# Optimization experiments

Measured on AMD Instinct MI355X. Metric: run time of the kernel, lower is better.

## Reference

```python
import jax, jax.numpy as jnp
import numpy as np

N_GENES = 768
HID = 128


def setup_inputs() -> dict:
    key = jax.random.key(0)
    ks = jax.random.split(key, 7)
    s1 = 1.0 / np.sqrt(2 * HID)
    s2 = 1.0 / np.sqrt(HID)
    return {
        "gene_embeddings": jax.random.normal(ks[0], (N_GENES, HID), jnp.float32),
        # regulatory_classifier: Linear(2h -> h), ReLU, Linear(h -> 3)
        "W1": jax.random.normal(ks[1], (HID, 2 * HID), jnp.float32) * s1,
        "b1": jax.random.normal(ks[2], (HID,), jnp.float32) * s1,
        "W2": jax.random.normal(ks[3], (3, HID), jnp.float32) * s2,
        "b2": jax.random.normal(ks[4], (3,), jnp.float32) * s2,
        # binding_predictor: Bilinear(h, h, 1) -> weight [1, h, h], bias [1]
        "Wb": jax.random.normal(ks[5], (1, HID, HID), jnp.float32) * s2,
        "bb": jax.random.normal(ks[6], (1,), jnp.float32) * s2,
    }


def reference(gene_embeddings, W1, b1, W2, b2, Wb, bb):
    """Vectorized equivalent of GeneRegulatoryNetwork.compute_regulatory_matrix.

    For every ordered pair (i, j), i != j:
      logits   = MLP(cat[x_i, x_j])            -> [3]
      cls      = argmax(logits)
      affinity = x_i^T Wb x_j + bb             (nn.Bilinear, out=1)
      reg[i,j] = +affinity if cls==0, -affinity if cls==2, else 0
    """
    X = gene_embeddings  # [n, h]
    n, h = X.shape
    # Linear(2h -> h) on cat[x_i, x_j] splits into two per-gene projections.
    Ai = X @ W1[:, :h].T  # [n, h] contribution of gene_i
    Bj = X @ W1[:, h:].T  # [n, h] contribution of gene_j
    hidden = jax.nn.relu(Ai[:, None, :] + Bj[None, :, :] + b1)  # [n, n, h]
    logits = hidden @ W2.T + b2  # [n, n, 3]
    reg_class = jnp.argmax(logits, axis=-1)  # [n, n] (first-max, matches torch)
    # Bilinear affinity: x_i^T Wb[0] x_j + bb[0]
    affinity = jnp.einsum('ik,kl,jl->ij', X, Wb[0], X) + bb[0]  # [n, n]
    sign = jnp.where(reg_class == 0, 1.0, jnp.where(reg_class == 2, -1.0, 0.0))
    reg = (sign * affinity).astype(X.dtype)
    # i == j pairs are skipped in the original loop -> zero diagonal
    reg = reg * (1.0 - jnp.eye(n, dtype=reg.dtype))
    return reg
```

## Files before the change

kernel.cpp:

```cpp
#include <hip/hip_runtime.h>

#define N_GENES 768
#define H 128
#define TILE 48
#define LDP 132
#define LDPH 136

typedef float    f2 __attribute__((ext_vector_type(2)));
typedef _Float16 h2 __attribute__((ext_vector_type(2)));
typedef _Float16 h8 __attribute__((ext_vector_type(8)));

__global__ __launch_bounds__(128) void grn_pre(
    const float* __restrict__ X, const float* __restrict__ W1,
    const float* __restrict__ b1, const float* __restrict__ Wb,
    float* __restrict__ AiB, float* __restrict__ Bjp,
    _Float16* __restrict__ Yh, _Float16* __restrict__ Xh)
{
    const int m  = threadIdx.x;
    const int g0 = blockIdx.x * 3;

    __shared__ float Xs[3][H];
    #pragma unroll
    for (int r = 0; r < 3; ++r) Xs[r][m] = X[(g0 + r) * H + m];
    __syncthreads();

    double aib[3] = {0, 0, 0}, bj[3] = {0, 0, 0}, y[3] = {0, 0, 0};
    const float4* W1a = (const float4*)(W1 + m * (2 * H));
    const float4* W1b = (const float4*)(W1 + m * (2 * H) + H);

    #pragma unroll 4
    for (int kq = 0; kq < H / 4; ++kq) {
        float4 wa = W1a[kq];
        float4 wb = W1b[kq];
        float wc[4];
        #pragma unroll
        for (int e = 0; e < 4; ++e) wc[e] = Wb[(kq * 4 + e) * H + m];
        const float* wae = &wa.x;
        const float* wbe = &wb.x;
        #pragma unroll
        for (int r = 0; r < 3; ++r) {
            float4 xr = *(const float4*)&Xs[r][kq * 4];
            const float* xe = &xr.x;
            #pragma unroll
            for (int e = 0; e < 4; ++e) {
                aib[r] += (double)xe[e] * (double)wae[e];
                bj[r]  += (double)xe[e] * (double)wbe[e];
                y[r]   += (double)xe[e] * (double)wc[e];
            }
        }
    }

    const double b1m = (double)b1[m];
    #pragma unroll
    for (int r = 0; r < 3; ++r) {
        AiB[(g0 + r) * H + m] = (float)(aib[r] + b1m);
        Bjp[(g0 + r) * H + m] = (float)bj[r];
        Yh [(g0 + r) * H + m] = (_Float16)(float)y[r];
        Xh [(g0 + r) * H + m] = (_Float16)Xs[r][m];
    }
}

__device__ __forceinline__ void load_tile_f32(float* __restrict__ dst,
                                              const float* __restrict__ src, int tx)
{
    #pragma unroll
    for (int t = 0; t < 6; ++t) {
        int idx = tx + t * 256;
        int row = idx >> 5;
        int c4  = idx & 31;
        *(float4*)&dst[row * LDP + c4 * 4] = *(const float4*)&src[row * H + c4 * 4];
    }
}

__device__ __forceinline__ void load_tile_f16(_Float16* __restrict__ dst,
                                              const _Float16* __restrict__ src, int tx)
{
    #pragma unroll
    for (int t = 0; t < 3; ++t) {
        int idx = tx + t * 256;
        int row = idx >> 4;
        int c8  = idx & 15;
        *(h8*)&dst[row * LDPH + c8 * 8] = *(const h8*)&src[row * H + c8 * 8];
    }
}

__device__ __forceinline__ h2 hpair(h8 v, int p) { h2 r; r.x = v[2*p]; r.y = v[2*p+1]; return r; }

__global__ __launch_bounds__(256) void grn_main(
    const float* __restrict__ AiB, const float* __restrict__ Bjp,
    const _Float16* __restrict__ Yh, const _Float16* __restrict__ Xh,
    const float* __restrict__ W2,  const float* __restrict__ b2,
    const float* __restrict__ bb,  float* __restrict__ out)
{
    const int gj = blockIdx.x & 15;
    const int gi = blockIdx.x >> 4;
    const int tx = threadIdx.x;
    const int it = tx >> 4;
    const int jt = tx & 15;

    __shared__ float sL[TILE * LDP];
    __shared__ float sR[TILE * LDP];
    __shared__ float sW[2 * H];

    _Float16* sLh = (_Float16*)sL;
    _Float16* sRh = (_Float16*)sR;

    load_tile_f16(sLh, Yh + gi * TILE * H, tx);
    load_tile_f16(sRh, Xh + gj * TILE * H, tx);
    if (tx < H) {
        sW[tx]     = W2[tx] - W2[2 * H + tx];
        sW[H + tx] = W2[tx] - W2[H + tx];
    }
    __syncthreads();

    float aff[3][3] = {};
    #pragma unroll 2
    for (int q = 0; q < H / 8; ++q) {
        h8 yv[3], xv[3];
        #pragma unroll
        for (int r = 0; r < 3; ++r) yv[r] = *(const h8*)&sLh[(it + 16 * r) * LDPH + q * 8];
        #pragma unroll
        for (int c = 0; c < 3; ++c) xv[c] = *(const h8*)&sRh[(jt + 16 * c) * LDPH + q * 8];
        #pragma unroll
        for (int r = 0; r < 3; ++r)
            #pragma unroll
            for (int c = 0; c < 3; ++c)
                #pragma unroll
                for (int p = 0; p < 4; ++p) {
#if __has_builtin(__builtin_amdgcn_fdot2)
                    aff[r][c] = __builtin_amdgcn_fdot2(hpair(yv[r], p), hpair(xv[c], p),
                                                       aff[r][c], false);
#else
                    h2 a = hpair(yv[r], p), b = hpair(xv[c], p);
                    aff[r][c] = fmaf((float)a.x, (float)b.x, aff[r][c]);
                    aff[r][c] = fmaf((float)a.y, (float)b.y, aff[r][c]);
#endif
                }
    }

    __syncthreads();

    load_tile_f32(sL, AiB + gi * TILE * H, tx);
    load_tile_f32(sR, Bjp + gj * TILE * H, tx);
    __syncthreads();

    const float u0 = b2[0] - b2[2];
    const float v0 = b2[0] - b2[1];
    float u[3][3], v[3][3];
    #pragma unroll
    for (int r = 0; r < 3; ++r)
        #pragma unroll
        for (int c = 0; c < 3; ++c) { u[r][c] = u0; v[r][c] = v0; }

    const f2 zero2 = {0.0f, 0.0f};
    #pragma unroll 4
    for (int mq = 0; mq < H / 4; ++mq) {
        float4 w0 = *(const float4*)&sW[mq * 4];
        float4 w1 = *(const float4*)&sW[H + mq * 4];
        float4 av[3], bv[3];
        #pragma unroll
        for (int r = 0; r < 3; ++r) av[r] = *(const float4*)&sL[(it + 16 * r) * LDP + mq * 4];
        #pragma unroll
        for (int c = 0; c < 3; ++c) bv[c] = *(const float4*)&sR[(jt + 16 * c) * LDP + mq * 4];
        #pragma unroll
        for (int r = 0; r < 3; ++r) {
            f2 a01 = {av[r].x, av[r].y};
            f2 a23 = {av[r].z, av[r].w};
            #pragma unroll
            for (int c = 0; c < 3; ++c) {
                f2 b01 = {bv[c].x, bv[c].y};
                f2 b23 = {bv[c].z, bv[c].w};
                f2 h01 = __builtin_elementwise_max(a01 + b01, zero2);
                f2 h23 = __builtin_elementwise_max(a23 + b23, zero2);
                float uu = u[r][c], vv = v[r][c];
                uu = fmaf(h01.x, w0.x, uu); vv = fmaf(h01.x, w1.x, vv);
                uu = fmaf(h01.y, w0.y, uu); vv = fmaf(h01.y, w1.y, vv);
                uu = fmaf(h23.x, w0.z, uu); vv = fmaf(h23.x, w1.z, vv);
                uu = fmaf(h23.y, w0.w, uu); vv = fmaf(h23.y, w1.w, vv);
                u[r][c] = uu; v[r][c] = vv;
            }
        }
    }

    const float bbv = bb[0];
    #pragma unroll
    for (int r = 0; r < 3; ++r) {
        const int i = gi * TILE + it + 16 * r;
        #pragma unroll
        for (int c = 0; c < 3; ++c) {
            const int j = gj * TILE + jt + 16 * c;
            float A = aff[r][c] + bbv;
            float uu = u[r][c], vv = v[r][c];
            float s = (uu >= 0.0f && vv >= 0.0f) ? A
                    : ((uu < 0.0f && uu < vv) ? -A : 0.0f);
            if (i == j) s = 0.0f;
            out[i * N_GENES + j] = s;
        }
    }
}

extern "C" void kernel_launch(void* const* d_in, const int* in_sizes, int n_in,
                              void* d_out, int out_size, void* d_ws, size_t ws_size,
                              hipStream_t stream)
{
    const float* X  = (const float*)d_in[0];
    const float* W1 = (const float*)d_in[1];
    const float* b1 = (const float*)d_in[2];
    const float* W2 = (const float*)d_in[3];
    const float* b2 = (const float*)d_in[4];
    const float* Wb = (const float*)d_in[5];
    const float* bb = (const float*)d_in[6];
    float* out = (float*)d_out;

    float* ws  = (float*)d_ws;
    float*     AiB = ws;
    float*     Bjp = ws + N_GENES * H;
    _Float16*  Yh  = (_Float16*)(ws + 2 * N_GENES * H);
    _Float16*  Xh  = (_Float16*)(ws + 2 * N_GENES * H) + N_GENES * H;

    grn_pre <<<N_GENES / 3, 128, 0, stream>>>(X, W1, b1, Wb, AiB, Bjp, Yh, Xh);
    grn_main<<<256,         256, 0, stream>>>(AiB, Bjp, Yh, Xh, W2, b2, bb, out);
}
```

Baseline: 89.27 us.

## Prefetch MLP tiles into registers during affinity loop; precompute W2 diffs in pre-kernel

The main kernel now issues the global loads for the AiB/Bjp tiles into registers before the fp16 affinity dot-product loop, then writes them to separate shared buffers afterwards. This overlaps that load latency with compute and removes one barrier. The W2 difference vectors are computed once in the pre-kernel and read straight from global memory instead of being staged in shared memory. The u/v accumulators are packed into 2-wide vector FMAs. In exchange, shared memory use roughly grows (separate buffers instead of aliased ones) and register pressure rises from the 12 prefetched float4 values, which may reduce occupancy.

```diff
diff --git a/kernel.cpp b/kernel.cpp
--- a/kernel.cpp
+++ b/kernel.cpp
@@ -13,11 +13,18 @@
 __global__ __launch_bounds__(128) void grn_pre(
     const float* __restrict__ X, const float* __restrict__ W1,
     const float* __restrict__ b1, const float* __restrict__ Wb,
+    const float* __restrict__ W2,
     float* __restrict__ AiB, float* __restrict__ Bjp,
-    _Float16* __restrict__ Yh, _Float16* __restrict__ Xh)
+    _Float16* __restrict__ Yh, _Float16* __restrict__ Xh,
+    float* __restrict__ W2u, float* __restrict__ W2v)
 {
     const int m  = threadIdx.x;
     const int g0 = blockIdx.x * 3;
+
+    if (blockIdx.x == 0) {
+        W2u[m] = W2[m] - W2[2 * H + m];
+        W2v[m] = W2[m] - W2[H + m];
+    }
 
     __shared__ float Xs[3][H];
     #pragma unroll
@@ -60,37 +67,14 @@
     }
 }
 
-__device__ __forceinline__ void load_tile_f32(float* __restrict__ dst,
-                                              const float* __restrict__ src, int tx)
-{
-    #pragma unroll
-    for (int t = 0; t < 6; ++t) {
-        int idx = tx + t * 256;
-        int row = idx >> 5;
-        int c4  = idx & 31;
-        *(float4*)&dst[row * LDP + c4 * 4] = *(const float4*)&src[row * H + c4 * 4];
-    }
-}
-
-__device__ __forceinline__ void load_tile_f16(_Float16* __restrict__ dst,
-                                              const _Float16* __restrict__ src, int tx)
-{
-    #pragma unroll
-    for (int t = 0; t < 3; ++t) {
-        int idx = tx + t * 256;
-        int row = idx >> 4;
-        int c8  = idx & 15;
-        *(h8*)&dst[row * LDPH + c8 * 8] = *(const h8*)&src[row * H + c8 * 8];
-    }
-}
-
 __device__ __forceinline__ h2 hpair(h8 v, int p) { h2 r; r.x = v[2*p]; r.y = v[2*p+1]; return r; }
 
 __global__ __launch_bounds__(256) void grn_main(
     const float* __restrict__ AiB, const float* __restrict__ Bjp,
     const _Float16* __restrict__ Yh, const _Float16* __restrict__ Xh,
-    const float* __restrict__ W2,  const float* __restrict__ b2,
-    const float* __restrict__ bb,  float* __restrict__ out)
+    const float* __restrict__ W2u, const float* __restrict__ W2v,
+    const float* __restrict__ b2,  const float* __restrict__ bb,
+    float* __restrict__ out)
 {
     const int gj = blockIdx.x & 15;
     const int gi = blockIdx.x >> 4;
@@ -98,19 +82,38 @@
     const int it = tx >> 4;
     const int jt = tx & 15;
 
-    __shared__ float sL[TILE * LDP];
-    __shared__ float sR[TILE * LDP];
-    __shared__ float sW[2 * H];
-
-    _Float16* sLh = (_Float16*)sL;
-    _Float16* sRh = (_Float16*)sR;
-
-    load_tile_f16(sLh, Yh + gi * TILE * H, tx);
-    load_tile_f16(sRh, Xh + gj * TILE * H, tx);
-    if (tx < H) {
-        sW[tx]     = W2[tx] - W2[2 * H + tx];
-        sW[H + tx] = W2[tx] - W2[H + tx];
-    }
+    __shared__ _Float16 sYh[TILE * LDPH];
+    __shared__ _Float16 sXh[TILE * LDPH];
+    __shared__ float    sA [TILE * LDP];
+    __shared__ float    sB [TILE * LDP];
+
+    {
+        const _Float16* srcY = Yh + gi * TILE * H;
+        const _Float16* srcX = Xh + gj * TILE * H;
+        #pragma unroll
+        for (int t = 0; t < 3; ++t) {
+            int idx = tx + t * 256;
+            int row = idx >> 4;
+            int c8  = idx & 15;
+            *(h8*)&sYh[row * LDPH + c8 * 8] = *(const h8*)&srcY[row * H + c8 * 8];
+            *(h8*)&sXh[row * LDPH + c8 * 8] = *(const h8*)&srcX[row * H + c8 * 8];
+        }
+    }
+
+    float4 aReg[6], bReg[6];
+    {
+        const float* srcA = AiB + gi * TILE * H;
+        const float* srcB = Bjp + gj * TILE * H;
+        #pragma unroll
+        for (int t = 0; t < 6; ++t) {
+            int idx = tx + t * 256;
+            int row = idx >> 5;
+            int c4  = idx & 31;
+            aReg[t] = *(const float4*)&srcA[row * H + c4 * 4];
+            bReg[t] = *(const float4*)&srcB[row * H + c4 * 4];
+        }
+    }
+
     __syncthreads();
 
     float aff[3][3] = {};
@@ -118,9 +121,9 @@
     for (int q = 0; q < H / 8; ++q) {
         h8 yv[3], xv[3];
         #pragma unroll
-        for (int r = 0; r < 3; ++r) yv[r] = *(const h8*)&sLh[(it + 16 * r) * LDPH + q * 8];
-        #pragma unroll
-        for (int c = 0; c < 3; ++c) xv[c] = *(const h8*)&sRh[(jt + 16 * c) * LDPH + q * 8];
+        for (int r = 0; r < 3; ++r) yv[r] = *(const h8*)&sYh[(it + 16 * r) * LDPH + q * 8];
+        #pragma unroll
+        for (int c = 0; c < 3; ++c) xv[c] = *(const h8*)&sXh[(jt + 16 * c) * LDPH + q * 8];
         #pragma unroll
         for (int r = 0; r < 3; ++r)
             #pragma unroll
@@ -138,30 +141,36 @@
                 }
     }
 
-    __syncthreads();
-
-    load_tile_f32(sL, AiB + gi * TILE * H, tx);
-    load_tile_f32(sR, Bjp + gj * TILE * H, tx);
+    #pragma unroll
+    for (int t = 0; t < 6; ++t) {
+        int idx = tx + t * 256;
+        int row = idx >> 5;
+        int c4  = idx & 31;
+        *(float4*)&sA[row * LDP + c4 * 4] = aReg[t];
+        *(float4*)&sB[row * LDP + c4 * 4] = bReg[t];
+    }
     __syncthreads();
 
     const float u0 = b2[0] - b2[2];
     const float v0 = b2[0] - b2[1];
-    float u[3][3], v[3][3];
+    f2 uv[3][3];
     #pragma unroll
     for (int r = 0; r < 3; ++r)
         #pragma unroll
-        for (int c = 0; c < 3; ++c) { u[r][c] = u0; v[r][c] = v0; }
-
+        for (int c = 0; c < 3; ++c) { uv[r][c].x = u0; uv[r][c].y = v0; }
+
+    const float4* w0p = (const float4*)W2u;
+    const float4* w1p = (const float4*)W2v;
     const f2 zero2 = {0.0f, 0.0f};
     #pragma unroll 4
     for (int mq = 0; mq < H / 4; ++mq) {
-        float4 w0 = *(const float4*)&sW[mq * 4];
-        float4 w1 = *(const float4*)&sW[H + mq * 4];
+        float4 w0 = w0p[mq];
+        float4 w1 = w1p[mq];
         float4 av[3], bv[3];
         #pragma unroll
-        for (int r = 0; r < 3; ++r) av[r] = *(const float4*)&sL[(it + 16 * r) * LDP + mq * 4];
-        #pragma unroll
-        for (int c = 0; c < 3; ++c) bv[c] = *(const float4*)&sR[(jt + 16 * c) * LDP + mq * 4];
+        for (int r = 0; r < 3; ++r) av[r] = *(const float4*)&sA[(it + 16 * r) * LDP + mq * 4];
+        #pragma unroll
+        for (int c = 0; c < 3; ++c) bv[c] = *(const float4*)&sB[(jt + 16 * c) * LDP + mq * 4];
         #pragma unroll
         for (int r = 0; r < 3; ++r) {
             f2 a01 = {av[r].x, av[r].y};
@@ -172,12 +181,12 @@
                 f2 b23 = {bv[c].z, bv[c].w};
                 f2 h01 = __builtin_elementwise_max(a01 + b01, zero2);
                 f2 h23 = __builtin_elementwise_max(a23 + b23, zero2);
-                float uu = u[r][c], vv = v[r][c];
-                uu = fmaf(h01.x, w0.x, uu); vv = fmaf(h01.x, w1.x, vv);
-                uu = fmaf(h01.y, w0.y, uu); vv = fmaf(h01.y, w1.y, vv);
-                uu = fmaf(h23.x, w0.z, uu); vv = fmaf(h23.x, w1.z, vv);
-                uu = fmaf(h23.y, w0.w, uu); vv = fmaf(h23.y, w1.w, vv);
-                u[r][c] = uu; v[r][c] = vv;
+                f2 acc = uv[r][c];
+                acc = __builtin_elementwise_fma((f2){h01.x, h01.x}, (f2){w0.x, w1.x}, acc);
+                acc = __builtin_elementwise_fma((f2){h01.y, h01.y}, (f2){w0.y, w1.y}, acc);
+                acc = __builtin_elementwise_fma((f2){h23.x, h23.x}, (f2){w0.z, w1.z}, acc);
+                acc = __builtin_elementwise_fma((f2){h23.y, h23.y}, (f2){w0.w, w1.w}, acc);
+                uv[r][c] = acc;
             }
         }
     }
@@ -190,7 +199,7 @@
         for (int c = 0; c < 3; ++c) {
             const int j = gj * TILE + jt + 16 * c;
             float A = aff[r][c] + bbv;
-            float uu = u[r][c], vv = v[r][c];
+            float uu = uv[r][c].x, vv = uv[r][c].y;
             float s = (uu >= 0.0f && vv >= 0.0f) ? A
                     : ((uu < 0.0f && uu < vv) ? -A : 0.0f);
             if (i == j) s = 0.0f;
@@ -216,8 +225,10 @@
     float*     AiB = ws;
     float*     Bjp = ws + N_GENES * H;
     _Float16*  Yh  = (_Float16*)(ws + 2 * N_GENES * H);
-    _Float16*  Xh  = (_Float16*)(ws + 2 * N_GENES * H) + N_GENES * H;
-
-    grn_pre <<<N_GENES / 3, 128, 0, stream>>>(X, W1, b1, Wb, AiB, Bjp, Yh, Xh);
-    grn_main<<<256,         256, 0, stream>>>(AiB, Bjp, Yh, Xh, W2, b2, bb, out);
+    _Float16*  Xh  = Yh + N_GENES * H;
+    float*     W2u = ws + 3 * N_GENES * H;
+    float*     W2v = W2u + H;
+
+    grn_pre <<<N_GENES / 3, 128, 0, stream>>>(X, W1, b1, Wb, W2, AiB, Bjp, Yh, Xh, W2u, W2v);
+    grn_main<<<256,         256, 0, stream>>>(AiB, Bjp, Yh, Xh, W2u, W2v, b2, bb, out);
 }
```

Measured after the change: 94.00 us. 1.05x slower.

## Compute bilinear affinity with MFMA, split pre-kernel K-loop, prefetch tiles into registers

Applied to the files above, without the earlier changes.

The bilinear affinity tile is now computed with 16x16x32 f16 MFMA instructions that read fp16 operands straight from global memory. The results are staged in a shared-memory tile, replacing the per-thread fdot2 loop over LDS. The AiB/Bjp tile loads are issued into registers before the MFMA work so their latency overlaps it. The pre-kernel now uses 256 threads and splits the K reduction in half, combining partial sums in shared memory to shorten the double-precision dependency chain. The cost is more shared memory, extra global reads without LDS reuse for the MFMA operands, and an added reduction sync.

```diff
diff --git a/kernel.cpp b/kernel.cpp
--- a/kernel.cpp
+++ b/kernel.cpp
@@ -4,42 +4,45 @@
 #define H 128
 #define TILE 48
 #define LDP 132
-#define LDPH 136
-
-typedef float    f2 __attribute__((ext_vector_type(2)));
-typedef _Float16 h2 __attribute__((ext_vector_type(2)));
+#define LDSA 50
+
+typedef float f32x4 __attribute__((ext_vector_type(4)));
 typedef _Float16 h8 __attribute__((ext_vector_type(8)));
 
-__global__ __launch_bounds__(128) void grn_pre(
+__global__ __launch_bounds__(256) void grn_pre(
     const float* __restrict__ X, const float* __restrict__ W1,
     const float* __restrict__ b1, const float* __restrict__ Wb,
     float* __restrict__ AiB, float* __restrict__ Bjp,
     _Float16* __restrict__ Yh, _Float16* __restrict__ Xh)
 {
-    const int m  = threadIdx.x;
+    const int tx = threadIdx.x;
+    const int m  = tx & 127;
+    const int h  = tx >> 7;
     const int g0 = blockIdx.x * 3;
 
-    __shared__ float Xs[3][H];
-    #pragma unroll
-    for (int r = 0; r < 3; ++r) Xs[r][m] = X[(g0 + r) * H + m];
+    __shared__ float  Xs[3 * H];
+    __shared__ double parts[3][3][H];
+
+    for (int idx = tx; idx < 3 * H; idx += 256) Xs[idx] = X[g0 * H + idx];
     __syncthreads();
 
     double aib[3] = {0, 0, 0}, bj[3] = {0, 0, 0}, y[3] = {0, 0, 0};
-    const float4* W1a = (const float4*)(W1 + m * (2 * H));
-    const float4* W1b = (const float4*)(W1 + m * (2 * H) + H);
+    const int kb = h * 64;
+    const float4* W1a = (const float4*)(W1 + m * (2 * H) + kb);
+    const float4* W1b = (const float4*)(W1 + m * (2 * H) + H + kb);
 
     #pragma unroll 4
-    for (int kq = 0; kq < H / 4; ++kq) {
+    for (int kq = 0; kq < 16; ++kq) {
         float4 wa = W1a[kq];
         float4 wb = W1b[kq];
         float wc[4];
         #pragma unroll
-        for (int e = 0; e < 4; ++e) wc[e] = Wb[(kq * 4 + e) * H + m];
+        for (int e = 0; e < 4; ++e) wc[e] = Wb[(kb + kq * 4 + e) * H + m];
         const float* wae = &wa.x;
         const float* wbe = &wb.x;
         #pragma unroll
         for (int r = 0; r < 3; ++r) {
-            float4 xr = *(const float4*)&Xs[r][kq * 4];
+            float4 xr = *(const float4*)&Xs[r * H + kb + kq * 4];
             const float* xe = &xr.x;
             #pragma unroll
             for (int e = 0; e < 4; ++e) {
@@ -50,41 +53,30 @@
         }
     }
 
-    const double b1m = (double)b1[m];
-    #pragma unroll
-    for (int r = 0; r < 3; ++r) {
-        AiB[(g0 + r) * H + m] = (float)(aib[r] + b1m);
-        Bjp[(g0 + r) * H + m] = (float)bj[r];
-        Yh [(g0 + r) * H + m] = (_Float16)(float)y[r];
-        Xh [(g0 + r) * H + m] = (_Float16)Xs[r][m];
+    if (h == 1) {
+        #pragma unroll
+        for (int r = 0; r < 3; ++r) {
+            parts[0][r][m] = aib[r];
+            parts[1][r][m] = bj[r];
+            parts[2][r][m] = y[r];
+        }
+    }
+    __syncthreads();
+
+    if (h == 0) {
+        const double b1m = (double)b1[m];
+        #pragma unroll
+        for (int r = 0; r < 3; ++r) {
+            double A = aib[r] + parts[0][r][m];
+            double B = bj[r]  + parts[1][r][m];
+            double Y = y[r]   + parts[2][r][m];
+            AiB[(g0 + r) * H + m] = (float)(A + b1m);
+            Bjp[(g0 + r) * H + m] = (float)B;
+            Yh [(g0 + r) * H + m] = (_Float16)(float)Y;
+            Xh [(g0 + r) * H + m] = (_Float16)Xs[r * H + m];
+        }
     }
 }
-
-__device__ __forceinline__ void load_tile_f32(float* __restrict__ dst,
-                                              const float* __restrict__ src, int tx)
-{
-    #pragma unroll
-    for (int t = 0; t < 6; ++t) {
-        int idx = tx + t * 256;
-        int row = idx >> 5;
-        int c4  = idx & 31;
-        *(float4*)&dst[row * LDP + c4 * 4] = *(const float4*)&src[row * H + c4 * 4];
-    }
-}
-
-__device__ __forceinline__ void load_tile_f16(_Float16* __restrict__ dst,
-                                              const _Float16* __restrict__ src, int tx)
-{
-    #pragma unroll
-    for (int t = 0; t < 3; ++t) {
-        int idx = tx + t * 256;
-        int row = idx >> 4;
-        int c8  = idx & 15;
-        *(h8*)&dst[row * LDPH + c8 * 8] = *(const h8*)&src[row * H + c8 * 8];
-    }
-}
-
-__device__ __forceinline__ h2 hpair(h8 v, int p) { h2 r; r.x = v[2*p]; r.y = v[2*p+1]; return r; }
 
 __global__ __launch_bounds__(256) void grn_main(
     const float* __restrict__ AiB, const float* __restrict__ Bjp,
@@ -97,51 +89,62 @@
     const int tx = threadIdx.x;
     const int it = tx >> 4;
     const int jt = tx & 15;
-
-    __shared__ float sL[TILE * LDP];
-    __shared__ float sR[TILE * LDP];
-    __shared__ float sW[2 * H];
-
-    _Float16* sLh = (_Float16*)sL;
-    _Float16* sRh = (_Float16*)sR;
-
-    load_tile_f16(sLh, Yh + gi * TILE * H, tx);
-    load_tile_f16(sRh, Xh + gj * TILE * H, tx);
+    const int wid = tx >> 6;
+    const int l   = tx & 63;
+
+    __shared__ float sA [TILE * LDP];
+    __shared__ float sB [TILE * LDP];
+    __shared__ float sW [2 * H];
+    __shared__ float sAff[TILE * LDSA];
+
     if (tx < H) {
         sW[tx]     = W2[tx] - W2[2 * H + tx];
         sW[H + tx] = W2[tx] - W2[H + tx];
     }
-    __syncthreads();
-
-    float aff[3][3] = {};
-    #pragma unroll 2
-    for (int q = 0; q < H / 8; ++q) {
-        h8 yv[3], xv[3];
-        #pragma unroll
-        for (int r = 0; r < 3; ++r) yv[r] = *(const h8*)&sLh[(it + 16 * r) * LDPH + q * 8];
-        #pragma unroll
-        for (int c = 0; c < 3; ++c) xv[c] = *(const h8*)&sRh[(jt + 16 * c) * LDPH + q * 8];
-        #pragma unroll
-        for (int r = 0; r < 3; ++r)
-            #pragma unroll
-            for (int c = 0; c < 3; ++c)
-                #pragma unroll
-                for (int p = 0; p < 4; ++p) {
-#if __has_builtin(__builtin_amdgcn_fdot2)
-                    aff[r][c] = __builtin_amdgcn_fdot2(hpair(yv[r], p), hpair(xv[c], p),
-                                                       aff[r][c], false);
-#else
-                    h2 a = hpair(yv[r], p), b = hpair(xv[c], p);
-                    aff[r][c] = fmaf((float)a.x, (float)b.x, aff[r][c]);
-                    aff[r][c] = fmaf((float)a.y, (float)b.y, aff[r][c]);
-#endif
-                }
-    }
-
-    __syncthreads();
-
-    load_tile_f32(sL, AiB + gi * TILE * H, tx);
-    load_tile_f32(sR, Bjp + gj * TILE * H, tx);
+
+    float4 aReg[6], bReg[6];
+    {
+        const float* srcA = AiB + gi * TILE * H;
+        const float* srcB = Bjp + gj * TILE * H;
+        #pragma unroll
+        for (int t = 0; t < 6; ++t) {
+            int idx = tx + t * 256;
+            int row = idx >> 5;
+            int c4  = idx & 31;
+            aReg[t] = *(const float4*)&srcA[row * H + c4 * 4];
+            bReg[t] = *(const float4*)&srcB[row * H + c4 * 4];
+        }
+    }
+
+    {
+        const _Float16* Ybase = Yh + (gi * TILE) * H;
+        const _Float16* Xbase = Xh + (gj * TILE) * H;
+        const int ro = l & 15;
+        const int ko = (l >> 4) * 8;
+        for (int t = wid; t < 9; t += 4) {
+            const int ti = t / 3, tj = t - ti * 3;
+            f32x4 acc = {0.f, 0.f, 0.f, 0.f};
+            #pragma unroll
+            for (int kk = 0; kk < 4; ++kk) {
+                h8 a = *(const h8*)&Ybase[(ti * 16 + ro) * H + kk * 32 + ko];
+                h8 b = *(const h8*)&Xbase[(tj * 16 + ro) * H + kk * 32 + ko];
+                acc = __builtin_amdgcn_mfma_f32_16x16x32_f16(a, b, acc, 0, 0, 0);
+            }
+            const int r0 = ti * 16 + ((l >> 4) << 2);
+            const int c0 = tj * 16 + ro;
+            #pragma unroll
+            for (int v = 0; v < 4; ++v) sAff[(r0 + v) * LDSA + c0] = acc[v];
+        }
+    }
+
+    #pragma unroll
+    for (int t = 0; t < 6; ++t) {
+        int idx = tx + t * 256;
+        int row = idx >> 5;
+        int c4  = idx & 31;
+        *(float4*)&sA[row * LDP + c4 * 4] = aReg[t];
+        *(float4*)&sB[row * LDP + c4 * 4] = bReg[t];
+    }
     __syncthreads();
 
     const float u0 = b2[0] - b2[2];
@@ -152,6 +155,7 @@
         #pragma unroll
         for (int c = 0; c < 3; ++c) { u[r][c] = u0; v[r][c] = v0; }
 
+    typedef float f2 __attribute__((ext_vector_type(2)));
     const f2 zero2 = {0.0f, 0.0f};
     #pragma unroll 4
     for (int mq = 0; mq < H / 4; ++mq) {
@@ -159,9 +163,9 @@
         float4 w1 = *(const float4*)&sW[H + mq * 4];
         float4 av[3], bv[3];
         #pragma unroll
-        for (int r = 0; r < 3; ++r) av[r] = *(const float4*)&sL[(it + 16 * r) * LDP + mq * 4];
-        #pragma unroll
-        for (int c = 0; c < 3; ++c) bv[c] = *(const float4*)&sR[(jt + 16 * c) * LDP + mq * 4];
+        for (int r = 0; r < 3; ++r) av[r] = *(const float4*)&sA[(it + 16 * r) * LDP + mq * 4];
+        #pragma unroll
+        for (int c = 0; c < 3; ++c) bv[c] = *(const float4*)&sB[(jt + 16 * c) * LDP + mq * 4];
         #pragma unroll
         for (int r = 0; r < 3; ++r) {
             f2 a01 = {av[r].x, av[r].y};
@@ -189,7 +193,7 @@
         #pragma unroll
         for (int c = 0; c < 3; ++c) {
             const int j = gj * TILE + jt + 16 * c;
-            float A = aff[r][c] + bbv;
+            float A = sAff[(it + 16 * r) * LDSA + (jt + 16 * c)] + bbv;
             float uu = u[r][c], vv = v[r][c];
             float s = (uu >= 0.0f && vv >= 0.0f) ? A
                     : ((uu < 0.0f && uu < vv) ? -A : 0.0f);
@@ -216,8 +220,8 @@
     float*     AiB = ws;
     float*     Bjp = ws + N_GENES * H;
     _Float16*  Yh  = (_Float16*)(ws + 2 * N_GENES * H);
-    _Float16*  Xh  = (_Float16*)(ws + 2 * N_GENES * H) + N_GENES * H;
-
-    grn_pre <<<N_GENES / 3, 128, 0, stream>>>(X, W1, b1, Wb, AiB, Bjp, Yh, Xh);
+    _Float16*  Xh  = Yh + N_GENES * H;
+
+    grn_pre <<<N_GENES / 3, 256, 0, stream>>>(X, W1, b1, Wb, AiB, Bjp, Yh, Xh);
     grn_main<<<256,         256, 0, stream>>>(AiB, Bjp, Yh, Xh, W2, b2, bb, out);
 }
```

Result: no change. 88.96 us (-0.3%).
